# Optimization experiments

Measured on AMD Instinct MI355X. Metric: run time of the kernel, lower is better.

Reference implementation:

```python
import jax, jax.numpy as jnp
import numpy as np
from jax import lax

H = W = 96
C = 3
N_PIX = H * W
N_PER_CLASS = 50   # min(size_sample_fg=100 -> shuffled to min_samples, size_sample_bg=50)
K = 5
THRESHOLD = 0.3
POS_WEIGHT = 100.0
CLEAN_THRESH = 0.6


def _sample_idx(key, valid_mask_flat, n):
    # Uniform random sample of n indices from valid positions (fixed-shape
    # replacement for tf.random.shuffle(tf.where(mask))[:n]).
    u = jax.random.uniform(key, (N_PIX,))
    score = jnp.where(valid_mask_flat, u, -1.0)
    _, idx = lax.top_k(score, n)
    return idx


def _pixel_features(img01):
    # img01: [H, W, C] in [0, 1]. Matches: reshape(img)/255 concat weighted positions.
    img_flat = img01.reshape(-1, C) / 255.0
    ii, jj = jnp.meshgrid(jnp.arange(H), jnp.arange(W), indexing='ij')
    pos = jnp.stack([ii, jj], axis=-1).reshape(-1, 2).astype(jnp.float32)
    pos = pos / jnp.array([H, W], jnp.float32) * POS_WEIGHT
    return jnp.concatenate([img_flat, pos], axis=1)  # [N_PIX, C+2]


def _process_image(img, key):
    # preprocess: (already 96x96x3) normalize & clip
    img_p = jnp.clip(img / 255.0, 0.0, 1.0)

    # extract_image_tf: clean image, pick fg/bg scribble pixels
    img_norm = img_p / jnp.max(img_p, axis=(0, 1), keepdims=True)
    cleaned = img_norm * (img_norm < CLEAN_THRESH).astype(jnp.float32)
    fg = jnp.any(cleaned > 0, axis=-1).reshape(-1)  # [N_PIX] bool
    bg = ~fg
    k_fg, k_bg = jax.random.split(key)
    fg_idx = _sample_idx(k_fg, fg, N_PER_CLASS)
    bg_idx = _sample_idx(k_bg, bg, N_PER_CLASS)

    # extract_features_tf
    feats_all = _pixel_features(img_p)                       # [N_PIX, 5]
    train_feats = jnp.concatenate([feats_all[fg_idx], feats_all[bg_idx]], axis=0)  # [100, 5]
    train_labels = jnp.concatenate([jnp.ones(N_PER_CLASS), jnp.zeros(N_PER_CLASS)])

    # segment_image_KNN_tf: standardize, brute-force cdist, top-k, label vote
    mean = jnp.mean(train_feats, axis=0)
    std = jnp.std(train_feats, axis=0)
    train_s = (train_feats - mean) / std                     # [100, 5]
    test_s = (feats_all - mean) / std                        # [N_PIX, 5]
    dist = jnp.sqrt(jnp.sum(jnp.square(test_s[:, None, :] - train_s[None, :, :]), axis=2))  # [N_PIX, 100]
    _, knn_idx = lax.top_k(-dist, K)                         # smallest-k distances
    probas = jnp.mean(train_labels[knn_idx], axis=1)         # [N_PIX]
    seg = (probas >= THRESHOLD).astype(jnp.int32).reshape(H, W)

    # mask original (preprocessed) image
    return jnp.where(seg[..., None] == 1, img_p, jnp.zeros_like(img_p))


def setup_inputs() -> dict:
    key = jax.random.key(0)
    images = jax.random.uniform(key, (32, H, W, C), dtype=jnp.float32)
    return {"images": images}


def reference(images):
    B = images.shape[0]
    keys = jax.random.split(jax.random.key(42), B)
    return jax.vmap(_process_image)(images, keys)
```

## Files before the change

kernel.cpp:

```cpp
#include <hip/hip_runtime.h>
#include <stdint.h>

#define NPIX 9216
#define NIMG 32

__device__ __forceinline__ uint32_t rotl32(uint32_t x, int d){ return (x<<d)|(x>>(32-d)); }

__device__ __forceinline__ void threefry(uint32_t k0, uint32_t k1, uint32_t x0, uint32_t x1,
                                         uint32_t &o0, uint32_t &o1){
  uint32_t ks2 = k0 ^ k1 ^ 0x1BD11BDAu;
  x0 += k0; x1 += k1;
  x0+=x1; x1=rotl32(x1,13); x1^=x0;
  x0+=x1; x1=rotl32(x1,15); x1^=x0;
  x0+=x1; x1=rotl32(x1,26); x1^=x0;
  x0+=x1; x1=rotl32(x1,6);  x1^=x0;
  x0+=k1; x1+=ks2+1u;
  x0+=x1; x1=rotl32(x1,17); x1^=x0;
  x0+=x1; x1=rotl32(x1,29); x1^=x0;
  x0+=x1; x1=rotl32(x1,16); x1^=x0;
  x0+=x1; x1=rotl32(x1,24); x1^=x0;
  x0+=ks2; x1+=k0+2u;
  x0+=x1; x1=rotl32(x1,13); x1^=x0;
  x0+=x1; x1=rotl32(x1,15); x1^=x0;
  x0+=x1; x1=rotl32(x1,26); x1^=x0;
  x0+=x1; x1=rotl32(x1,6);  x1^=x0;
  x0+=k0; x1+=k1+3u;
  x0+=x1; x1=rotl32(x1,17); x1^=x0;
  x0+=x1; x1=rotl32(x1,29); x1^=x0;
  x0+=x1; x1=rotl32(x1,16); x1^=x0;
  x0+=x1; x1=rotl32(x1,24); x1^=x0;
  x0+=k1; x1+=ks2+4u;
  x0+=x1; x1=rotl32(x1,13); x1^=x0;
  x0+=x1; x1=rotl32(x1,15); x1^=x0;
  x0+=x1; x1=rotl32(x1,26); x1^=x0;
  x0+=x1; x1=rotl32(x1,6);  x1^=x0;
  x0+=ks2; x1+=k0+5u;
  o0=x0; o1=x1;
}

__device__ __forceinline__ float clip01_div255(float x){
  return fminf(fmaxf(x/255.0f, 0.0f), 1.0f);
}

__global__ __launch_bounds__(1024) void kprep(const float* __restrict__ in,
                                              float* __restrict__ ts2g,
                                              float* __restrict__ meanstd){
#pragma clang fp contract(off)
  int img = blockIdx.x;
  int tid = threadIdx.x;

  __shared__ uint32_t vvL[NPIX];
  __shared__ uint64_t cand[2][1024];
  __shared__ int      ncA[2];
  __shared__ int      hist[2][129];
  __shared__ int      bbinL[2];
  __shared__ float    cmaxL[3];
  __shared__ float    wred[3][16];
  __shared__ int      tIdx[100];
  __shared__ float    feat[100][5];
  __shared__ float    mv[5], sv[5];

  if(tid<258) ((int*)hist)[tid]=0;
  if(tid<2)   ncA[tid]=0;

  const float* p = in + (size_t)img*NPIX*3;
  const float4* ip4 = (const float4*)p;

  float4 rv[3][3];
  float m0=0.f, m1=0.f, m2=0.f;
#pragma unroll
  for(int k=0;k<3;k++){
    int g = k*1024 + tid;
    if(g < 2304){
      float4 v0 = ip4[3*g+0], v1 = ip4[3*g+1], v2 = ip4[3*g+2];
      rv[k][0]=v0; rv[k][1]=v1; rv[k][2]=v2;
      m0 = fmaxf(m0, fmaxf(fmaxf(clip01_div255(v0.x), clip01_div255(v0.w)),
                           fmaxf(clip01_div255(v1.z), clip01_div255(v2.y))));
      m1 = fmaxf(m1, fmaxf(fmaxf(clip01_div255(v0.y), clip01_div255(v1.x)),
                           fmaxf(clip01_div255(v1.w), clip01_div255(v2.z))));
      m2 = fmaxf(m2, fmaxf(fmaxf(clip01_div255(v0.z), clip01_div255(v1.y)),
                           fmaxf(clip01_div255(v2.x), clip01_div255(v2.w))));
    }
  }
  for(int off=32; off>0; off>>=1){
    m0 = fmaxf(m0, __shfl_down(m0,off));
    m1 = fmaxf(m1, __shfl_down(m1,off));
    m2 = fmaxf(m2, __shfl_down(m2,off));
  }
  { int lane = tid & 63, wv = tid >> 6;
    if(lane==0){ wred[0][wv]=m0; wred[1][wv]=m1; wred[2][wv]=m2; } }
  __syncthreads();
  if(tid<3){
    float m = wred[tid][0];
    for(int w=1;w<16;w++) m = fmaxf(m, wred[tid][w]);
    cmaxL[tid]=m;
  }
  __syncthreads();
  float c0=cmaxL[0], c1=cmaxL[1], c2=cmaxL[2];

  uint32_t ik0, ik1; threefry(0u, 42u, 0u, (uint32_t)img, ik0, ik1);
  uint32_t sf0, sf1; threefry(ik0, ik1, 0u, 0u, sf0, sf1);
  uint32_t sb0, sb1; threefry(ik0, ik1, 0u, 1u, sb0, sb1);

  auto score_px = [&](int px, float pa, float pb, float pc){
    float a  = clip01_div255(pa)/c0;
    float bb = clip01_div255(pb)/c1;
    float c  = clip01_div255(pc)/c2;
    bool fg = (a>0.f && a<0.6f) || (bb>0.f && bb<0.6f) || (c>0.f && c<0.6f);
    uint32_t k0 = fg ? sf0 : sb0, k1 = fg ? sf1 : sb1;
    uint32_t r1, r2; threefry(k0, k1, 0u, (uint32_t)px, r1, r2);
    uint32_t vv = ((r1 ^ r2) >> 9) + 1u;
    vvL[px] = vv | (fg ? 0x80000000u : 0u);
    atomicAdd(&hist[fg?0:1][vv>>16], 1);
  };
#pragma unroll
  for(int k=0;k<3;k++){
    int g = k*1024 + tid;
    if(g < 2304){
      float4 v0=rv[k][0], v1=rv[k][1], v2=rv[k][2];
      int pb = g*4;
      score_px(pb+0, v0.x, v0.y, v0.z);
      score_px(pb+1, v0.w, v1.x, v1.y);
      score_px(pb+2, v1.z, v1.w, v2.x);
      score_px(pb+3, v2.y, v2.z, v2.w);
    }
  }
  __syncthreads();

  if(tid<128){
    int cls = tid>>6, l = tid&63;
    int h0 = hist[cls][2*l];
    int h1 = hist[cls][2*l+1];
    int h128 = hist[cls][128];
    int S = h0 + h1;
    for(int off=1; off<64; off<<=1){
      int o = __shfl_down(S, off);
      if(l + off < 64) S += o;
    }
    int ss0 = S + h128;
    int ss1 = S - h0 + h128;
    int cd = -1;
    if(ss0 >= 50) cd = 2*l;
    if(ss1 >= 50) cd = 2*l+1;
    if(l==63 && h128 >= 50) cd = 128;
    for(int off=32; off>0; off>>=1){
      int o = __shfl_down(cd, off);
      cd = o > cd ? o : cd;
    }
    if(l==0) bbinL[cls] = cd;
  }
  __syncthreads();

  {
    int bb0 = bbinL[0], bb1 = bbinL[1];
    for(int k=0;k<9;k++){
      int px = k*1024 + tid;
      uint32_t w = vvL[px];
      int cls = (w & 0x80000000u) ? 0 : 1;
      uint32_t vv = w & 0x7FFFFFFFu;
      int bb = cls ? bb1 : bb0;
      if((int)(vv>>16) >= bb){
        int pos = atomicAdd(&ncA[cls],1);
        if(pos < 1024)
          cand[cls][pos] = ((uint64_t)vv << 14) | (uint64_t)(16383 - px);
      }
    }
  }
  __syncthreads();

  {
    int cls = (tid >= 512);
    int lt  = tid & 511;
    int m = ncA[cls]; if(m > 1024) m = 1024;
    const uint64_t* C = cand[cls];
    for(int c=lt; c<m; c+=512){
      uint64_t kk = C[c];
      int r = 0, j = 0;
      while(j < m){
        int je = j+64 < m ? j+64 : m;
        for(; j<je; j++) r += (C[j] > kk);
        if(r >= 50) break;
      }
      if(r < 50) tIdx[cls*50 + r] = 16383 - (int)(kk & 16383u);
    }
  }
  __syncthreads();

  for(int cls=0; cls<2; cls++){
    if(bbinL[cls] == -1){
      uint32_t want = (cls==0) ? 0x80000000u : 0u;
      if(tid==0){
        int m = ncA[cls];
        int need = 50 - m, r = m;
        for(int px=0; px<NPIX && need>0; px++){
          if((vvL[px] & 0x80000000u) != want){ tIdx[cls*50 + r] = px; r++; need--; }
        }
      }
      __syncthreads();
    }
  }

  if(tid<100){
    int pp = tIdx[tid];
    int i=pp/96, j=pp-i*96;
    const float* px = in + ((size_t)img*NPIX + pp)*3;
    for(int c=0;c<3;c++){
      float ip=clip01_div255(px[c]);
      feat[tid][c]=ip/255.0f;
    }
    feat[tid][3]=((float)i/96.0f)*100.0f;
    feat[tid][4]=((float)j/96.0f)*100.0f;
  }
  __syncthreads();
  if(tid<5){
    float s=0.f;
    for(int r=0;r<100;r++) s=s+feat[r][tid];
    float mu=s/100.0f; mv[tid]=mu;
    float v=0.f;
    for(int r=0;r<100;r++){ float d=feat[r][tid]-mu; float q=d*d; v=v+q; }
    sv[tid]=sqrtf(v/100.0f);
  }
  __syncthreads();
  if(tid<100){
    float r0=(feat[tid][0]-mv[0])/sv[0];
    float r1=(feat[tid][1]-mv[1])/sv[1];
    float r2=(feat[tid][2]-mv[2])/sv[2];
    float r3=(feat[tid][3]-mv[3])/sv[3];
    float r4=(feat[tid][4]-mv[4])/sv[4];
    float* dst = ts2g + img*600 + (tid>>1)*12 + (tid&1);
    dst[0]=r0; dst[2]=r1; dst[4]=r2; dst[6]=r3; dst[8]=r4;
  }
  if(tid<5)       meanstd[img*10+tid]=mv[tid];
  else if(tid<10) meanstd[img*10+tid]=sv[tid-5];
}

__global__ __launch_bounds__(256) void kknn(const float* __restrict__ in,
                                            const float* __restrict__ ts2g,
                                            const float* __restrict__ meanstd,
                                            float* __restrict__ out){
#pragma clang fp contract(off)
  int b     = blockIdx.x;
  int img   = b / 36;
  int chunk = b % 36;
  int tid   = threadIdx.x;

  __shared__ float    mv[5], sv[5];
  __shared__ __attribute__((aligned(16))) float ts2[600];
  __shared__ __attribute__((aligned(16))) float pix[768];

  if(tid<150) ((float4*)ts2)[tid] = ((const float4*)(ts2g + img*600))[tid];
  if(tid>=192 && tid<197) mv[tid-192]=meanstd[img*10+(tid-192)];
  if(tid>=224 && tid<229) sv[tid-224]=meanstd[img*10+5+(tid-224)];
  {
    const float4* cb4 = (const float4*)(in + ((size_t)img*NPIX + (size_t)chunk*256)*3);
    if(tid<192) ((float4*)pix)[tid] = cb4[tid];
  }
  __syncthreads();

  int p = chunk*256+tid;
  int i=p/96, j=p-i*96;
  float ip0=clip01_div255(pix[tid*3+0]);
  float ip1=clip01_div255(pix[tid*3+1]);
  float ip2=clip01_div255(pix[tid*3+2]);
  float t0,t1,t2,t3,t4;
  {
    float f0=ip0/255.0f, f1=ip1/255.0f, f2=ip2/255.0f;
    float f3=((float)i/96.0f)*100.0f, f4=((float)j/96.0f)*100.0f;
    t0=(f0-mv[0])/sv[0]; t1=(f1-mv[1])/sv[1]; t2=(f2-mv[2])/sv[2];
    t3=(f3-mv[3])/sv[3]; t4=(f4-mv[4])/sv[4];
  }

  float a0x=1e30f,a0y=1e30f, a1x=1e30f,a1y=1e30f;
#pragma unroll 5
  for(int pr=0;pr<25;pr++){
    const float* tp = &ts2[pr*12];
    float4 qA = *(const float4*)(tp);
    float4 qB = *(const float4*)(tp+4);
    float2 qC = *(const float2*)(tp+8);
    float sx, sy;
    { float dx=t0-qA.x, dy=t0-qA.y; sx=dx*dx; sy=dy*dy; }
    { float dx=t1-qA.z, dy=t1-qA.w; float wx=dx*dx, wy=dy*dy; sx=sx+wx; sy=sy+wy; }
    { float dx=t2-qB.x, dy=t2-qB.y; float wx=dx*dx, wy=dy*dy; sx=sx+wx; sy=sy+wy; }
    { float dx=t3-qB.z, dy=t3-qB.w; float wx=dx*dx, wy=dy*dy; sx=sx+wx; sy=sy+wy; }
    { float dx=t4-qC.x, dy=t4-qC.y; float wx=dx*dx, wy=dy*dy; sx=sx+wx; sy=sy+wy; }
    float tx=fmaxf(a0x,sx), ty=fmaxf(a0y,sy);
    a0x=fminf(a0x,sx);      a0y=fminf(a0y,sy);
    a1x=fminf(a1x,tx);      a1y=fminf(a1y,ty);
  }
  float a1 = fmaxf(fminf(a0x,a1y), fminf(a1x,a0y));

  float b0x=1e30f,b0y=1e30f, b1x=1e30f,b1y=1e30f;
  float b2x=1e30f,b2y=1e30f, b3x=1e30f,b3y=1e30f;
#pragma unroll 5
  for(int pr=25;pr<50;pr++){
    const float* tp = &ts2[pr*12];
    float4 qA = *(const float4*)(tp);
    float4 qB = *(const float4*)(tp+4);
    float2 qC = *(const float2*)(tp+8);
    float sx, sy;
    { float dx=t0-qA.x, dy=t0-qA.y; sx=dx*dx; sy=dy*dy; }
    { float dx=t1-qA.z, dy=t1-qA.w; float wx=dx*dx, wy=dy*dy; sx=sx+wx; sy=sy+wy; }
    { float dx=t2-qB.x, dy=t2-qB.y; float wx=dx*dx, wy=dy*dy; sx=sx+wx; sy=sy+wy; }
    { float dx=t3-qB.z, dy=t3-qB.w; float wx=dx*dx, wy=dy*dy; sx=sx+wx; sy=sy+wy; }
    { float dx=t4-qC.x, dy=t4-qC.y; float wx=dx*dx, wy=dy*dy; sx=sx+wx; sy=sy+wy; }
    float u0x=fmaxf(b0x,sx), u0y=fmaxf(b0y,sy);
    b0x=fminf(b0x,sx);       b0y=fminf(b0y,sy);
    float u1x=fmaxf(b1x,u0x), u1y=fmaxf(b1y,u0y);
    b1x=fminf(b1x,u0x);       b1y=fminf(b1y,u0y);
    float u2x=fmaxf(b2x,u1x), u2y=fmaxf(b2y,u1y);
    b2x=fminf(b2x,u1x);       b2y=fminf(b2y,u1y);
    b3x=fminf(b3x,u2x);       b3y=fminf(b3y,u2y);
  }
  float l0=fminf(b0x,b3y), l1=fminf(b1x,b2y), l2=fminf(b2x,b1y), l3=fminf(b3x,b0y);
  float b3 = fmaxf(fmaxf(l0,l1), fmaxf(l2,l3));

  bool seg = sqrtf(a1) <= sqrtf(b3);
  __syncthreads();
  pix[tid*3+0]=seg?ip0:0.f;
  pix[tid*3+1]=seg?ip1:0.f;
  pix[tid*3+2]=seg?ip2:0.f;
  __syncthreads();
  float4* ob4 = (float4*)(out + ((size_t)img*NPIX + (size_t)chunk*256)*3);
  if(tid<192) ob4[tid] = ((float4*)pix)[tid];
}

extern "C" void kernel_launch(void* const* d_in, const int* in_sizes, int n_in,
                              void* d_out, int out_size, void* d_ws, size_t ws_size,
                              hipStream_t stream) {
  const float* in = (const float*)d_in[0];
  float* out = (float*)d_out;
  float* ts2g    = (float*)d_ws;
  float* meanstd = (float*)((char*)d_ws + 76800);

  kprep<<<32,   1024, 0, stream>>>(in, ts2g, meanstd);
  kknn <<<1152, 256,  0, stream>>>(in, ts2g, meanstd, out);
}
```

Before: 108.4 us.

## Split per-image prep kernel into parallel strip scoring and finalize kernels

The single 32-block prep kernel is split in two. A 256-block scoring kernel has eight blocks per image: each recomputes the channel max, scores one strip of pixels with threefry, writes the tagged scores to global memory and emits partial histograms. A finalize kernel then sums the histograms and selects the samples. The aim is to spread the threefry-heavy scoring across more of the GPU than 32 blocks can use. In exchange it adds a kernel launch, global round trips for scores and histograms, and an eightfold redundant read of each image for the max.

```diff
diff --git a/kernel.cpp b/kernel.cpp
--- a/kernel.cpp
+++ b/kernel.cpp
@@ -3,6 +3,7 @@
 
 #define NPIX 9216
 #define NIMG 32
+#define STRIP 1152
 
 __device__ __forceinline__ uint32_t rotl32(uint32_t x, int d){ return (x<<d)|(x>>(32-d)); }
 
@@ -42,59 +43,47 @@
   return fminf(fmaxf(x/255.0f, 0.0f), 1.0f);
 }
 
-__global__ __launch_bounds__(1024) void kprep(const float* __restrict__ in,
-                                              float* __restrict__ ts2g,
-                                              float* __restrict__ meanstd){
+__global__ __launch_bounds__(256) void kscore(const float* __restrict__ in,
+                                              uint32_t* __restrict__ vvG,
+                                              int* __restrict__ histPart){
 #pragma clang fp contract(off)
-  int img = blockIdx.x;
+  int b   = blockIdx.x;
+  int img = b >> 3, sub = b & 7;
   int tid = threadIdx.x;
 
-  __shared__ uint32_t vvL[NPIX];
-  __shared__ uint64_t cand[2][1024];
-  __shared__ int      ncA[2];
-  __shared__ int      hist[2][129];
-  __shared__ int      bbinL[2];
-  __shared__ float    cmaxL[3];
-  __shared__ float    wred[3][16];
-  __shared__ int      tIdx[100];
-  __shared__ float    feat[100][5];
-  __shared__ float    mv[5], sv[5];
-
-  if(tid<258) ((int*)hist)[tid]=0;
-  if(tid<2)   ncA[tid]=0;
+  __shared__ int   hist[258];
+  __shared__ float wred[3][4];
+  __shared__ float cmaxL[3];
+
+  for(int i=tid;i<258;i+=256) hist[i]=0;
 
   const float* p = in + (size_t)img*NPIX*3;
-  const float4* ip4 = (const float4*)p;
-
-  float4 rv[3][3];
-  float m0=0.f, m1=0.f, m2=0.f;
-#pragma unroll
-  for(int k=0;k<3;k++){
-    int g = k*1024 + tid;
-    if(g < 2304){
-      float4 v0 = ip4[3*g+0], v1 = ip4[3*g+1], v2 = ip4[3*g+2];
-      rv[k][0]=v0; rv[k][1]=v1; rv[k][2]=v2;
-      m0 = fmaxf(m0, fmaxf(fmaxf(clip01_div255(v0.x), clip01_div255(v0.w)),
-                           fmaxf(clip01_div255(v1.z), clip01_div255(v2.y))));
-      m1 = fmaxf(m1, fmaxf(fmaxf(clip01_div255(v0.y), clip01_div255(v1.x)),
-                           fmaxf(clip01_div255(v1.w), clip01_div255(v2.z))));
-      m2 = fmaxf(m2, fmaxf(fmaxf(clip01_div255(v0.z), clip01_div255(v1.y)),
-                           fmaxf(clip01_div255(v2.x), clip01_div255(v2.w))));
-    }
-  }
-  for(int off=32; off>0; off>>=1){
-    m0 = fmaxf(m0, __shfl_down(m0,off));
-    m1 = fmaxf(m1, __shfl_down(m1,off));
-    m2 = fmaxf(m2, __shfl_down(m2,off));
-  }
-  { int lane = tid & 63, wv = tid >> 6;
-    if(lane==0){ wred[0][wv]=m0; wred[1][wv]=m1; wred[2][wv]=m2; } }
-  __syncthreads();
-  if(tid<3){
-    float m = wred[tid][0];
-    for(int w=1;w<16;w++) m = fmaxf(m, wred[tid][w]);
-    cmaxL[tid]=m;
-  }
+
+  {
+    const float4* ip4 = (const float4*)p;
+    float m0=0.f, m1=0.f, m2=0.f;
+    for(int k=0;k<27;k++){
+      int i4 = k*256 + tid;
+      float4 v = ip4[i4];
+      float e0=clip01_div255(v.x), e1=clip01_div255(v.y),
+            e2=clip01_div255(v.z), e3=clip01_div255(v.w);
+      int b3 = i4 % 3;
+      float cb = fmaxf(e0,e3);
+      m0 = fmaxf(m0, b3==0 ? cb : (b3==1 ? e2 : e1));
+      m1 = fmaxf(m1, b3==0 ? e1 : (b3==1 ? cb : e2));
+      m2 = fmaxf(m2, b3==0 ? e2 : (b3==1 ? e1 : cb));
+    }
+    for(int off=32; off>0; off>>=1){
+      m0 = fmaxf(m0, __shfl_down(m0,off));
+      m1 = fmaxf(m1, __shfl_down(m1,off));
+      m2 = fmaxf(m2, __shfl_down(m2,off));
+    }
+    int lane = tid & 63, wv = tid >> 6;
+    if(lane==0){ wred[0][wv]=m0; wred[1][wv]=m1; wred[2][wv]=m2; }
+  }
+  __syncthreads();
+  if(tid<3) cmaxL[tid] = fmaxf(fmaxf(wred[tid][0],wred[tid][1]),
+                               fmaxf(wred[tid][2],wred[tid][3]));
   __syncthreads();
   float c0=cmaxL[0], c1=cmaxL[1], c2=cmaxL[2];
 
@@ -102,22 +91,25 @@
   uint32_t sf0, sf1; threefry(ik0, ik1, 0u, 0u, sf0, sf1);
   uint32_t sb0, sb1; threefry(ik0, ik1, 0u, 1u, sb0, sb1);
 
-  auto score_px = [&](int px, float pa, float pb, float pc){
+  uint32_t* vstrip = vvG + (size_t)img*NPIX + (size_t)sub*STRIP;
+  const float4* sp4 = (const float4*)(p + (size_t)sub*STRIP*3);
+  auto score_px = [&](int pxl, float pa, float pb, float pc){
     float a  = clip01_div255(pa)/c0;
     float bb = clip01_div255(pb)/c1;
     float c  = clip01_div255(pc)/c2;
     bool fg = (a>0.f && a<0.6f) || (bb>0.f && bb<0.6f) || (c>0.f && c<0.6f);
     uint32_t k0 = fg ? sf0 : sb0, k1 = fg ? sf1 : sb1;
-    uint32_t r1, r2; threefry(k0, k1, 0u, (uint32_t)px, r1, r2);
+    uint32_t gi = (uint32_t)(sub*STRIP + pxl);
+    uint32_t r1, r2; threefry(k0, k1, 0u, gi, r1, r2);
     uint32_t vv = ((r1 ^ r2) >> 9) + 1u;
-    vvL[px] = vv | (fg ? 0x80000000u : 0u);
-    atomicAdd(&hist[fg?0:1][vv>>16], 1);
+    vstrip[pxl] = vv | (fg ? 0x80000000u : 0u);
+    atomicAdd(&hist[(fg?0:129) + (int)(vv>>16)], 1);
   };
 #pragma unroll
-  for(int k=0;k<3;k++){
-    int g = k*1024 + tid;
-    if(g < 2304){
-      float4 v0=rv[k][0], v1=rv[k][1], v2=rv[k][2];
+  for(int w=0;w<2;w++){
+    int g = w*256 + tid;
+    if(g < 288){
+      float4 v0 = sp4[3*g+0], v1 = sp4[3*g+1], v2 = sp4[3*g+2];
       int pb = g*4;
       score_px(pb+0, v0.x, v0.y, v0.z);
       score_px(pb+1, v0.w, v1.x, v1.y);
@@ -126,12 +118,39 @@
     }
   }
   __syncthreads();
+  for(int i=tid;i<258;i+=256) histPart[(size_t)b*258 + i] = hist[i];
+}
+
+__global__ __launch_bounds__(1024) void kfin(const float* __restrict__ in,
+                                             const uint32_t* __restrict__ vvG,
+                                             const int* __restrict__ histPart,
+                                             float* __restrict__ ts2g,
+                                             float* __restrict__ meanstd){
+#pragma clang fp contract(off)
+  int img = blockIdx.x;
+  int tid = threadIdx.x;
+
+  __shared__ int      hist2[258];
+  __shared__ uint64_t cand[2][1024];
+  __shared__ int      ncA[2], bbinL[2];
+  __shared__ int      tIdx[100];
+  __shared__ float    feat[100][5];
+  __shared__ float    mv[5], sv[5];
+
+  if(tid<2) ncA[tid]=0;
+  if(tid<258){
+    int s=0;
+#pragma unroll
+    for(int s8=0;s8<8;s8++) s += histPart[((size_t)img*8+s8)*258 + tid];
+    hist2[tid]=s;
+  }
+  __syncthreads();
 
   if(tid<128){
     int cls = tid>>6, l = tid&63;
-    int h0 = hist[cls][2*l];
-    int h1 = hist[cls][2*l+1];
-    int h128 = hist[cls][128];
+    int h0 = hist2[cls*129 + 2*l];
+    int h1 = hist2[cls*129 + 2*l+1];
+    int h128 = hist2[cls*129 + 128];
     int S = h0 + h1;
     for(int off=1; off<64; off<<=1){
       int o = __shfl_down(S, off);
@@ -151,11 +170,12 @@
   }
   __syncthreads();
 
+  const uint32_t* vp = vvG + (size_t)img*NPIX;
   {
     int bb0 = bbinL[0], bb1 = bbinL[1];
     for(int k=0;k<9;k++){
       int px = k*1024 + tid;
-      uint32_t w = vvL[px];
+      uint32_t w = vp[px];
       int cls = (w & 0x80000000u) ? 0 : 1;
       uint32_t vv = w & 0x7FFFFFFFu;
       int bb = cls ? bb1 : bb0;
@@ -193,7 +213,7 @@
         int m = ncA[cls];
         int need = 50 - m, r = m;
         for(int px=0; px<NPIX && need>0; px++){
-          if((vvL[px] & 0x80000000u) != want){ tIdx[cls*50 + r] = px; r++; need--; }
+          if((vp[px] & 0x80000000u) != want){ tIdx[cls*50 + r] = px; r++; need--; }
         }
       }
       __syncthreads();
@@ -329,9 +349,12 @@
                               hipStream_t stream) {
   const float* in = (const float*)d_in[0];
   float* out = (float*)d_out;
-  float* ts2g    = (float*)d_ws;
-  float* meanstd = (float*)((char*)d_ws + 76800);
-
-  kprep<<<32,   1024, 0, stream>>>(in, ts2g, meanstd);
-  kknn <<<1152, 256,  0, stream>>>(in, ts2g, meanstd, out);
-}
+  uint32_t* vvG     = (uint32_t*)d_ws;
+  int*      histPart= (int*)((char*)d_ws + 1179648);
+  float*    ts2g    = (float*)((char*)d_ws + 1443840);
+  float*    meanstd = (float*)((char*)d_ws + 1520640);
+
+  kscore<<<256,  256,  0, stream>>>(in, vvG, histPart);
+  kfin  <<<32,   1024, 0, stream>>>(in, vvG, histPart, ts2g, meanstd);
+  kknn  <<<1152, 256,  0, stream>>>(in, ts2g, meanstd, out);
+}
```

Measured after the change: 116.1 us. +7.1%, slower.
